# Kernel optimization log

Hardware: AMD Instinct MI355X
Metric: run time of the kernel (lower is better)

The kernel has to match this reference:

```python
import jax, jax.numpy as jnp
import numpy as np

NUM_EMBEDDINGS = 1024
EMBEDDING_DIM = 256
COMMITMENT_COST = 0.25


def setup_inputs() -> dict:
    key = jax.random.key(0)
    k1, k2 = jax.random.split(key)
    inputs = jax.random.normal(k1, (65536, EMBEDDING_DIM), dtype=jnp.float32)
    # original init: uniform(-1/K, 1/K)
    embeddings = jax.random.uniform(
        k2, (NUM_EMBEDDINGS, EMBEDDING_DIM), dtype=jnp.float32,
        minval=-1.0 / NUM_EMBEDDINGS, maxval=1.0 / NUM_EMBEDDINGS)
    return {"inputs": inputs, "embeddings": embeddings}


def reference(inputs, embeddings):
    D = embeddings.shape[1]
    flat = inputs.reshape(-1, D)                                   # [N, D]
    distances = (jnp.sum(flat ** 2, axis=1, keepdims=True)
                 + jnp.sum(embeddings ** 2, axis=1)
                 - 2.0 * flat @ embeddings.T)
    indices = jnp.argmin(distances, axis=1)                        # [N]
    # one-hot @ codebook == direct gather
    quantized = embeddings[indices].reshape(inputs.shape)
    q_loss = jnp.mean((jax.lax.stop_gradient(quantized) - inputs) ** 2)
    e_loss = jnp.mean((quantized - jax.lax.stop_gradient(inputs)) ** 2)
    loss = q_loss + COMMITMENT_COST * e_loss
    # straight-through estimator
    quantized = inputs + jax.lax.stop_gradient(quantized - inputs)
    return quantized, loss
```

## Files before the change

kernel.cpp:

```cpp
#include <hip/hip_runtime.h>
#include <stdint.h>

#define N_ROWS 65536
#define K_CODES 1024
#define DIM 256

typedef unsigned int uint;
typedef unsigned short ushort;

#define WS_LOSS_OFF  0
#define WS_ENORM_OFF 4096
#define WS_E8_OFF    8192

typedef __attribute__((ext_vector_type(4))) float f32x4;

#define XSCALE 16.0f
#define ESCALE 256.0f
#define SCORE_C 4.8828125e-4f

__device__ __forceinline__ uint pack4_fp8(float a, float b, float c, float d) {
    uint r = 0;
    r = __builtin_amdgcn_cvt_pk_fp8_f32(a, b, r, false);
    r = __builtin_amdgcn_cvt_pk_fp8_f32(c, d, r, true);
    return r;
}
__device__ __forceinline__ void gload_lds16(const void* g, void* l) {
    __builtin_amdgcn_global_load_lds(
        (const __attribute__((address_space(1))) void*)g,
        (__attribute__((address_space(3))) void*)l, 16, 0, 0);
}

__global__ __launch_bounds__(256) void vq_prep(const float* __restrict__ E,
                                               unsigned char* __restrict__ E8,
                                               float* __restrict__ enorm) {
    int id = blockIdx.x * 256 + threadIdx.x;
    int code = id >> 6, c4 = id & 63;
    float4 v = *reinterpret_cast<const float4*>(E + (size_t)code * DIM + c4 * 4);
    uint p = pack4_fp8(v.x * ESCALE, v.y * ESCALE, v.z * ESCALE, v.w * ESCALE);
    *reinterpret_cast<uint*>(E8 + (size_t)code * 256 + c4 * 4) = p;

    float s = v.x * v.x + v.y * v.y + v.z * v.z + v.w * v.w;
    #pragma unroll
    for (int m = 32; m >= 1; m >>= 1) s += __shfl_down(s, m, 64);
    if (c4 == 0) enorm[code] = s;
}

__global__ __launch_bounds__(256, 2) void vq_main(const float* __restrict__ X,
                                                  const unsigned char* __restrict__ E8,
                                                  const float* __restrict__ enorm,
                                                  const float* __restrict__ E,
                                                  float* __restrict__ out,
                                                  float* __restrict__ lossAcc) {
    __shared__ __align__(16) unsigned char bsm[2 * 16384];
    __shared__ float enormLds[1024];
    __shared__ float xnormLds[128];
    __shared__ int   bcLds[128];
    __shared__ float lossSh;

    const int tid = threadIdx.x;
    const int lane = tid & 63;
    const int w = tid >> 6;
    const int cl = lane & 15;
    const int kq = lane >> 4;
    const int row0 = blockIdx.x * 128;

    auto stageB = [&](int tile, int buf) {
        unsigned char* dst = bsm + buf * 16384;
        const unsigned char* src = E8 + (size_t)(tile * 64) * 256;
        #pragma unroll
        for (int j = 0; j < 4; ++j) {
            int o = j * 4096 + tid * 16;
            int rr = o >> 8;
            int cb = (o & 255) ^ ((rr & 7) << 4);
            gload_lds16(src + rr * 256 + cb, dst + o);
        }
    };

    stageB(0, 0);

    reinterpret_cast<float4*>(enormLds)[tid] =
        reinterpret_cast<const float4*>(enorm)[tid];
    if (tid == 0) lossSh = 0.f;

    long aF[2][8];
    #pragma unroll
    for (int m = 0; m < 2; ++m) {
        const float* rp = X + (size_t)(row0 + w * 32 + m * 16 + cl) * DIM;
        float s = 0.f;
        #pragma unroll
        for (int ks = 0; ks < 8; ++ks) {
            float4 v0 = *reinterpret_cast<const float4*>(rp + ks * 32 + kq * 8);
            float4 v1 = *reinterpret_cast<const float4*>(rp + ks * 32 + kq * 8 + 4);
            uint lo = pack4_fp8(v0.x * XSCALE, v0.y * XSCALE,
                                v0.z * XSCALE, v0.w * XSCALE);
            uint hi = pack4_fp8(v1.x * XSCALE, v1.y * XSCALE,
                                v1.z * XSCALE, v1.w * XSCALE);
            aF[m][ks] = (long)(((unsigned long long)hi << 32) | lo);
            s = fmaf(v0.x, v0.x, s); s = fmaf(v0.y, v0.y, s);
            s = fmaf(v0.z, v0.z, s); s = fmaf(v0.w, v0.w, s);
            s = fmaf(v1.x, v1.x, s); s = fmaf(v1.y, v1.y, s);
            s = fmaf(v1.z, v1.z, s); s = fmaf(v1.w, v1.w, s);
        }
        s += __shfl_xor(s, 16, 64);
        s += __shfl_xor(s, 32, 64);
        if (kq == 0) xnormLds[w * 32 + m * 16 + cl] = s;
    }

    float best[2][4];
    int bcode[2][4];
    #pragma unroll
    for (int m = 0; m < 2; ++m)
        #pragma unroll
        for (int rr = 0; rr < 4; ++rr) { best[m][rr] = 3.4e38f; bcode[m][rr] = 0; }

    for (int t = 0; t < 16; ++t) {
        __syncthreads();
        if (t < 15) stageB(t + 1, (t + 1) & 1);

        const unsigned char* bb = bsm + (t & 1) * 16384;
        float en[4];
        #pragma unroll
        for (int n = 0; n < 4; ++n) en[n] = enormLds[t * 64 + n * 16 + cl];

        f32x4 acc[2][4];
        #pragma unroll
        for (int m = 0; m < 2; ++m)
            #pragma unroll
            for (int n = 0; n < 4; ++n) {
                f32x4 z = {0.f, 0.f, 0.f, 0.f};
                acc[m][n] = z;
            }

        __builtin_amdgcn_s_setprio(1);
        #pragma unroll
        for (int ks = 0; ks < 8; ++ks) {
            #pragma unroll
            for (int n = 0; n < 4; ++n) {
                long bf = *reinterpret_cast<const long*>(
                    bb + (size_t)(n * 16 + cl) * 256
                       + ((ks * 32 + kq * 8) ^ ((cl & 7) << 4)));
                #pragma unroll
                for (int m = 0; m < 2; ++m)
                    acc[m][n] = __builtin_amdgcn_mfma_f32_16x16x32_fp8_fp8(
                        aF[m][ks], bf, acc[m][n], 0, 0, 0);
            }
        }
        __builtin_amdgcn_s_setprio(0);

        #pragma unroll
        for (int n = 0; n < 4; ++n) {
            int codeN = t * 64 + n * 16 + cl;
            #pragma unroll
            for (int m = 0; m < 2; ++m)
                #pragma unroll
                for (int rr = 0; rr < 4; ++rr) {
                    float sc = fmaf(-SCORE_C, acc[m][n][rr], en[n]);
                    if (sc < best[m][rr]) { best[m][rr] = sc; bcode[m][rr] = codeN; }
                }
        }
    }

    float lsum = 0.f;
    #pragma unroll
    for (int m = 0; m < 2; ++m)
        #pragma unroll
        for (int rr = 0; rr < 4; ++rr) {
            float b = best[m][rr];
            int cc = bcode[m][rr];
            #pragma unroll
            for (int mask = 1; mask < 16; mask <<= 1) {
                float ob = __shfl_xor(b, mask, 64);
                int oc = __shfl_xor(cc, mask, 64);
                if (ob < b || (ob == b && oc < cc)) { b = ob; cc = oc; }
            }
            if (cl == 0) {
                int row_l = w * 32 + m * 16 + kq * 4 + rr;
                bcLds[row_l] = cc;
                lsum += xnormLds[row_l] + b;
            }
        }
    lsum += __shfl_xor(lsum, 16, 64);
    lsum += __shfl_xor(lsum, 32, 64);
    if (lane == 0) atomicAdd(&lossSh, lsum);
    __syncthreads();

    #pragma unroll 4
    for (int i = 0; i < 32; ++i) {
        int g = i * 256 + tid;
        int rr = g >> 6, c4 = g & 63;
        int code = bcLds[rr];
        float4 q = *reinterpret_cast<const float4*>(E + (size_t)code * DIM + c4 * 4);
        *reinterpret_cast<float4*>(out + (size_t)(row0 + rr) * DIM + c4 * 4) = q;
    }
    if (tid == 0) atomicAdd(lossAcc, lossSh);
}

__global__ void vq_finalize(const float* __restrict__ lossAcc,
                            float* __restrict__ out) {
    out[(size_t)N_ROWS * DIM] = 1.25f * lossAcc[0] / (float)((size_t)N_ROWS * DIM);
}

extern "C" void kernel_launch(void* const* d_in, const int* in_sizes, int n_in,
                              void* d_out, int out_size, void* d_ws, size_t ws_size,
                              hipStream_t stream) {
    const float* X = (const float*)d_in[0];
    const float* E = (const float*)d_in[1];
    float* out = (float*)d_out;

    char* ws = (char*)d_ws;
    float* lossAcc = (float*)(ws + WS_LOSS_OFF);
    float* enorm = (float*)(ws + WS_ENORM_OFF);
    unsigned char* E8 = (unsigned char*)(ws + WS_E8_OFF);

    hipMemsetAsync(lossAcc, 0, 4, stream);
    vq_prep<<<256, 256, 0, stream>>>(E, E8, enorm);
    vq_main<<<N_ROWS / 128, 256, 0, stream>>>(X, E8, enorm, E, out, lossAcc);
    vq_finalize<<<1, 1, 0, stream>>>(lossAcc, out);
}
```

Measured before the change: 64.40 us.

## Use 16x16x128 scaled FP8 MFMA with larger codebook tiles

Replaces the 16x16x32 FP8 MFMA with the gfx950 scaled 16x16x128 f8f6f4 MFMA, using unit scales. This cuts the MFMA instruction count fourfold and uses wider 16-byte LDS fragment loads. It also doubles the codebook tile to 128 codes per stage, halving the number of barriers. The final output stores become nontemporal. The cost is twice the LDS (64KB for B), which may limit occupancy, plus more accumulator registers.

```diff
diff --git a/kernel.cpp b/kernel.cpp
--- a/kernel.cpp
+++ b/kernel.cpp
@@ -13,10 +13,13 @@
 #define WS_E8_OFF    8192
 
 typedef __attribute__((ext_vector_type(4))) float f32x4;
+typedef __attribute__((ext_vector_type(4))) int   i32x4;
+typedef __attribute__((ext_vector_type(8))) int   i32x8;
 
 #define XSCALE 16.0f
 #define ESCALE 256.0f
 #define SCORE_C 4.8828125e-4f
+#define SCALE1 0x7F7F7F7Fu
 
 __device__ __forceinline__ uint pack4_fp8(float a, float b, float c, float d) {
     uint r = 0;
@@ -51,7 +54,7 @@
                                                   const float* __restrict__ E,
                                                   float* __restrict__ out,
                                                   float* __restrict__ lossAcc) {
-    __shared__ __align__(16) unsigned char bsm[2 * 16384];
+    __shared__ __align__(16) unsigned char bsm[2 * 32768];
     __shared__ float enormLds[1024];
     __shared__ float xnormLds[128];
     __shared__ int   bcLds[128];
@@ -63,12 +66,13 @@
     const int cl = lane & 15;
     const int kq = lane >> 4;
     const int row0 = blockIdx.x * 128;
+    const int key = (cl & 7) << 4;
 
     auto stageB = [&](int tile, int buf) {
-        unsigned char* dst = bsm + buf * 16384;
-        const unsigned char* src = E8 + (size_t)(tile * 64) * 256;
-        #pragma unroll
-        for (int j = 0; j < 4; ++j) {
+        unsigned char* dst = bsm + buf * 32768;
+        const unsigned char* src = E8 + (size_t)(tile * 128) * 256;
+        #pragma unroll
+        for (int j = 0; j < 8; ++j) {
             int o = j * 4096 + tid * 16;
             int rr = o >> 8;
             int cb = (o & 255) ^ ((rr & 7) << 4);
@@ -82,24 +86,26 @@
         reinterpret_cast<const float4*>(enorm)[tid];
     if (tid == 0) lossSh = 0.f;
 
-    long aF[2][8];
+    i32x8 aF[2][2];
     #pragma unroll
     for (int m = 0; m < 2; ++m) {
         const float* rp = X + (size_t)(row0 + w * 32 + m * 16 + cl) * DIM;
         float s = 0.f;
         #pragma unroll
-        for (int ks = 0; ks < 8; ++ks) {
-            float4 v0 = *reinterpret_cast<const float4*>(rp + ks * 32 + kq * 8);
-            float4 v1 = *reinterpret_cast<const float4*>(rp + ks * 32 + kq * 8 + 4);
-            uint lo = pack4_fp8(v0.x * XSCALE, v0.y * XSCALE,
-                                v0.z * XSCALE, v0.w * XSCALE);
-            uint hi = pack4_fp8(v1.x * XSCALE, v1.y * XSCALE,
-                                v1.z * XSCALE, v1.w * XSCALE);
-            aF[m][ks] = (long)(((unsigned long long)hi << 32) | lo);
-            s = fmaf(v0.x, v0.x, s); s = fmaf(v0.y, v0.y, s);
-            s = fmaf(v0.z, v0.z, s); s = fmaf(v0.w, v0.w, s);
-            s = fmaf(v1.x, v1.x, s); s = fmaf(v1.y, v1.y, s);
-            s = fmaf(v1.z, v1.z, s); s = fmaf(v1.w, v1.w, s);
+        for (int ks = 0; ks < 2; ++ks) {
+            const float* p = rp + ks * 128 + kq * 32;
+            uint u[8];
+            #pragma unroll
+            for (int q = 0; q < 8; ++q) {
+                float4 v = *reinterpret_cast<const float4*>(p + q * 4);
+                u[q] = pack4_fp8(v.x * XSCALE, v.y * XSCALE,
+                                 v.z * XSCALE, v.w * XSCALE);
+                s = fmaf(v.x, v.x, s); s = fmaf(v.y, v.y, s);
+                s = fmaf(v.z, v.z, s); s = fmaf(v.w, v.w, s);
+            }
+            i32x8 f = {(int)u[0], (int)u[1], (int)u[2], (int)u[3],
+                       (int)u[4], (int)u[5], (int)u[6], (int)u[7]};
+            aF[m][ks] = f;
         }
         s += __shfl_xor(s, 16, 64);
         s += __shfl_xor(s, 32, 64);
@@ -113,43 +119,48 @@
         #pragma unroll
         for (int rr = 0; rr < 4; ++rr) { best[m][rr] = 3.4e38f; bcode[m][rr] = 0; }
 
-    for (int t = 0; t < 16; ++t) {
+    for (int t = 0; t < 8; ++t) {
         __syncthreads();
-        if (t < 15) stageB(t + 1, (t + 1) & 1);
-
-        const unsigned char* bb = bsm + (t & 1) * 16384;
-        float en[4];
-        #pragma unroll
-        for (int n = 0; n < 4; ++n) en[n] = enormLds[t * 64 + n * 16 + cl];
-
-        f32x4 acc[2][4];
+        if (t < 7) stageB(t + 1, (t + 1) & 1);
+
+        const unsigned char* bb = bsm + (t & 1) * 32768;
+        float en[8];
+        #pragma unroll
+        for (int n = 0; n < 8; ++n) en[n] = enormLds[t * 128 + n * 16 + cl];
+
+        f32x4 acc[2][8];
         #pragma unroll
         for (int m = 0; m < 2; ++m)
             #pragma unroll
-            for (int n = 0; n < 4; ++n) {
+            for (int n = 0; n < 8; ++n) {
                 f32x4 z = {0.f, 0.f, 0.f, 0.f};
                 acc[m][n] = z;
             }
 
         __builtin_amdgcn_s_setprio(1);
         #pragma unroll
-        for (int ks = 0; ks < 8; ++ks) {
-            #pragma unroll
-            for (int n = 0; n < 4; ++n) {
-                long bf = *reinterpret_cast<const long*>(
-                    bb + (size_t)(n * 16 + cl) * 256
-                       + ((ks * 32 + kq * 8) ^ ((cl & 7) << 4)));
+        for (int ks = 0; ks < 2; ++ks) {
+            #pragma unroll
+            for (int n = 0; n < 8; ++n) {
+                const unsigned char* rbase = bb + (size_t)(n * 16 + cl) * 256;
+                int l0 = ks * 128 + kq * 32;
+                i32x4 lo = *reinterpret_cast<const i32x4*>(rbase + (l0 ^ key));
+                i32x4 hi = *reinterpret_cast<const i32x4*>(rbase + ((l0 + 16) ^ key));
+                i32x8 bf = __builtin_shufflevector(lo, hi, 0, 1, 2, 3, 4, 5, 6, 7);
                 #pragma unroll
                 for (int m = 0; m < 2; ++m)
-                    acc[m][n] = __builtin_amdgcn_mfma_f32_16x16x32_fp8_fp8(
-                        aF[m][ks], bf, acc[m][n], 0, 0, 0);
+                    acc[m][n] = __builtin_amdgcn_mfma_scale_f32_16x16x128_f8f6f4(
+                        aF[m][ks], bf, acc[m][n],
+                        0, 0,
+                        0, SCALE1,
+                        0, SCALE1);
             }
         }
         __builtin_amdgcn_s_setprio(0);
 
         #pragma unroll
-        for (int n = 0; n < 4; ++n) {
-            int codeN = t * 64 + n * 16 + cl;
+        for (int n = 0; n < 8; ++n) {
+            int codeN = t * 128 + n * 16 + cl;
             #pragma unroll
             for (int m = 0; m < 2; ++m)
                 #pragma unroll
@@ -189,8 +200,9 @@
         int g = i * 256 + tid;
         int rr = g >> 6, c4 = g & 63;
         int code = bcLds[rr];
-        float4 q = *reinterpret_cast<const float4*>(E + (size_t)code * DIM + c4 * 4);
-        *reinterpret_cast<float4*>(out + (size_t)(row0 + rr) * DIM + c4 * 4) = q;
+        f32x4 q = *reinterpret_cast<const f32x4*>(E + (size_t)code * DIM + c4 * 4);
+        __builtin_nontemporal_store(q,
+            reinterpret_cast<f32x4*>(out + (size_t)(row0 + rr) * DIM + c4 * 4));
     }
     if (tid == 0) atomicAdd(lossAcc, lossSh);
 }
```

After: 54.74 us. -15.0%, faster.
